# Optimization experiments

Measured on AMD Instinct MI355X. Metric: run time of the kernel, lower is better.

## Reference

```python
import jax, jax.numpy as jnp
import numpy as np
from math import sqrt

D_MODEL, D_COND, N_HEADS = 512, 768, 8
B, H, W, L_COND = 8, 64, 64, 256


def setup_inputs() -> dict:
    key = jax.random.key(0)
    ks = jax.random.split(key, 7)
    return {
        "image": jax.random.normal(ks[0], (B, D_MODEL, H, W), jnp.float32),
        "cond": jax.random.normal(ks[1], (B, L_COND, D_COND), jnp.float32),
        "attention_mask": jnp.zeros((B, H * W, L_COND), jnp.float32),
        "Wq": jax.random.normal(ks[2], (D_MODEL, D_MODEL), jnp.float32) * 0.02,
        "Wk": jax.random.normal(ks[3], (D_MODEL, D_COND), jnp.float32) * 0.02,
        "Wv": jax.random.normal(ks[4], (D_MODEL, D_COND), jnp.float32) * 0.02,
        "Wo": jax.random.normal(ks[5], (D_MODEL, D_MODEL), jnp.float32) * 0.02,
        "bo": jnp.zeros((D_MODEL,), jnp.float32),
    }


def reference(image, cond, attention_mask, Wq, Wk, Wv, Wo, bo):
    b, d, h, w = image.shape
    L = h * w
    n = N_HEADS
    dh = d // n
    scale = sqrt(dh)
    # b d h w -> b l d
    x = image.reshape(b, d, L).transpose(0, 2, 1)
    # projections (torch Linear: y = x @ W.T), split heads: b l (n dh) -> b n l dh
    q = (x @ Wq.T).reshape(b, L, n, dh).transpose(0, 2, 1, 3)
    k = (cond @ Wk.T).reshape(b, -1, n, dh).transpose(0, 2, 1, 3)
    v = (cond @ Wv.T).reshape(b, -1, n, dh).transpose(0, 2, 1, 3)
    attn = jnp.einsum("bnqd,bnkd->bnqk", q, k) / scale
    attn = attn + attention_mask[:, None]  # b 1 L L_cond
    p = jax.nn.softmax(attn, axis=-1)
    o = jnp.einsum("bnqk,bnkd->bnqd", p, v)  # b n L dh
    # b n (h w) dh -> b (n dh) h w
    o = o.transpose(0, 1, 3, 2).reshape(b, d, h, w)
    # 1x1 conv == per-pixel linear over channels
    out = jnp.einsum("oc,bchw->bohw", Wo, o) + bo[None, :, None, None]
    return out
```

## Files before the change

kernel.cpp:

```cpp
#include <hip/hip_runtime.h>

typedef __bf16 bf16x8 __attribute__((ext_vector_type(8)));
typedef float f32x4 __attribute__((ext_vector_type(4)));
typedef short s4 __attribute__((ext_vector_type(4)));
typedef unsigned short ush;

#define DEV __device__ __forceinline__


DEV ush f2bf(float x){
  union { float f; unsigned u; } v; v.f = x;
  unsigned r = v.u + 0x7FFFu + ((v.u >> 16) & 1u);
  return (ush)(r >> 16);
}

DEV short bfcast(float x){
  union { __bf16 h; short s; } cv; cv.h = (__bf16)x; return cv.s;
}

DEV void gload_lds16(const ush* g, ush* l){
  __builtin_amdgcn_global_load_lds(
      (const __attribute__((address_space(1))) unsigned int*)g,
      (__attribute__((address_space(3))) unsigned int*)l, 16, 0, 0);
}

__global__ __launch_bounds__(256) void tc_kernel(const float* __restrict__ img, ush* __restrict__ xT){
  __shared__ float tile[32][33];
  const int b = blockIdx.z;
  const int l0 = blockIdx.x << 5, c0 = blockIdx.y << 5;
  const int tx = threadIdx.x & 31, ty = threadIdx.x >> 5;
  const float* src = img + ((size_t)b*512 + c0)*4096 + l0;
  #pragma unroll
  for (int i = 0; i < 32; i += 8) tile[ty+i][tx] = src[(size_t)(ty+i)*4096 + tx];
  __syncthreads();
  ush* dst = xT + ((size_t)b*4096 + l0)*512 + c0;
  #pragma unroll
  for (int i = 0; i < 32; i += 8) dst[(size_t)(ty+i)*512 + tx] = f2bf(tile[tx][ty+i]);
}

__global__ __launch_bounds__(256) void cvt_kernel(const float* c0,const float* c1,const float* c2,
                                                  const float* c3,const float* c4,
                                                  ush* o0, ush* o1, ush* o2, ush* o3, ush* o4){
  const int N0=1572864, N1=262144, N2=393216, N3=393216, N4=262144;
  const int stride = gridDim.x * blockDim.x;
  for (int i = blockIdx.x*blockDim.x + threadIdx.x; i < N0+N1+N2+N3+N4; i += stride){
    int j = i; const float* s; ush* d;
    if (j < N0){ s=c0; d=o0; }
    else { j-=N0; if (j<N1){s=c1;d=o1;}
      else { j-=N1; if (j<N2){s=c2;d=o2;}
        else { j-=N2; if (j<N3){s=c3;d=o3;} else { j-=N3; s=c4; d=o4; } } } }
    d[j] = f2bf(s[j]);
  }
}

DEV void gemm_core(const ush* __restrict__ Ag, long long a_row0, int lda,
                   const ush* __restrict__ Bg, long long b_row0, int ldb,
                   int K, ush* As, ush* Bs, f32x4 acc[4][4])
{
  const int t = threadIdx.x;
  const int lane = t & 63;
  const int wid = t >> 6, wr = wid >> 1, wc = wid & 1;
  #pragma unroll
  for (int mt=0;mt<4;mt++)
    #pragma unroll
    for (int nt=0;nt<4;nt++) acc[mt][nt] = f32x4{0.f,0.f,0.f,0.f};

  const int nk = K >> 6;
  for (int kt = 0; kt < nk; ++kt){
    const int k0 = kt << 6;
    #pragma unroll
    for (int r = 0; r < 4; ++r){
      int idx = (r<<8) + t;
      int row = idx >> 3, slot = idx & 7;
      gload_lds16(Ag + (a_row0 + row)*(long long)lda + k0 + ((slot ^ (row&7))<<3), As + idx*8);
    }
    #pragma unroll
    for (int r = 0; r < 4; ++r){
      int idx = (r<<8) + t;
      int row = idx >> 3, slot = idx & 7;
      gload_lds16(Bg + (b_row0 + row)*(long long)ldb + k0 + ((slot ^ (row&7))<<3), Bs + idx*8);
    }
    __syncthreads();
    #pragma unroll
    for (int kk = 0; kk < 2; ++kk){
      bf16x8 af[4], bfv[4];
      #pragma unroll
      for (int mt=0;mt<4;mt++){
        int row = (wr<<6) + (mt<<4) + (lane & 15);
        int byte = (row<<7) + (kk<<6) + ((lane>>4)<<4);
        byte ^= (row & 7) << 4;
        af[mt] = *(const bf16x8*)((const char*)As + byte);
      }
      #pragma unroll
      for (int nt=0;nt<4;nt++){
        int row = (wc<<6) + (nt<<4) + (lane & 15);
        int byte = (row<<7) + (kk<<6) + ((lane>>4)<<4);
        byte ^= (row & 7) << 4;
        bfv[nt] = *(const bf16x8*)((const char*)Bs + byte);
      }
      #pragma unroll
      for (int mt=0;mt<4;mt++)
        #pragma unroll
        for (int nt=0;nt<4;nt++)
          acc[mt][nt] = __builtin_amdgcn_mfma_f32_16x16x32_bf16(af[mt], bfv[nt], acc[mt][nt], 0,0,0);
    }
    __syncthreads();
  }
}

__global__ __launch_bounds__(256,2) void qproj_kernel(const ush* __restrict__ xT, const ush* __restrict__ Wqb,
                                                      ush* __restrict__ Qg){
  __shared__ ush As[8192], Bs[8192];
  f32x4 acc[4][4];
  const int nb = blockIdx.x & 3, mb = blockIdx.x >> 2;
  gemm_core(xT, (long long)mb*128, 512, Wqb, (long long)nb*128, 512, 512, As, Bs, acc);
  const int lane = threadIdx.x & 63, wid = threadIdx.x >> 6, wr = wid>>1, wc = wid&1;
  #pragma unroll
  for (int mt=0;mt<4;mt++)
    #pragma unroll
    for (int nt=0;nt<4;nt++)
      #pragma unroll
      for (int r=0;r<4;r++){
        int m = mb*128 + (wr<<6) + (mt<<4) + ((lane>>4)<<2) + r;
        int n = (nb<<7) + (wc<<6) + (nt<<4) + (lane&15);
        int bb = m >> 12, l = m & 4095, hh = n >> 6, dh = n & 63;
        Qg[(((size_t)(bb*8 + hh)*4096 + l)<<6) + dh] = f2bf(acc[mt][nt][r] * 0.125f);
      }
}

__global__ __launch_bounds__(256,2) void kvproj_kernel(const ush* __restrict__ cb, const ush* __restrict__ Wkb,
                                                       const ush* __restrict__ Wvb, ush* __restrict__ Kg,
                                                       ush* __restrict__ Vt){
  __shared__ ush As[8192], Bs[8192];
  f32x4 acc[4][4];
  const int which = blockIdx.z;
  const int nb = blockIdx.x & 3, mb = blockIdx.x >> 2;
  gemm_core(cb, (long long)mb*128, 768, which ? Wvb : Wkb, (long long)nb*128, 768, 768, As, Bs, acc);
  const int lane = threadIdx.x & 63, wid = threadIdx.x >> 6, wr = wid>>1, wc = wid&1;
  #pragma unroll
  for (int mt=0;mt<4;mt++)
    #pragma unroll
    for (int nt=0;nt<4;nt++)
      #pragma unroll
      for (int r=0;r<4;r++){
        int m = mb*128 + (wr<<6) + (mt<<4) + ((lane>>4)<<2) + r;
        int n = (nb<<7) + (wc<<6) + (nt<<4) + (lane&15);
        int bb = m >> 8, j = m & 255;
        ush val = f2bf(acc[mt][nt][r]);
        if (!which) Kg[(((size_t)(bb*256 + j))<<9) + n] = val;
        else { int hh = n>>6, dh = n&63; Vt[(((size_t)((bb*8+hh)*64 + dh))<<8) + j] = val; }
      }
}

__global__ __launch_bounds__(1024,3) void attn_kernel(const ush* __restrict__ Qg, const ush* __restrict__ Kg,
                                                      const ush* __restrict__ Vg, const float* __restrict__ mask,
                                                      ush* __restrict__ Oc){
  extern __shared__ char smem[];
  ush* Ks = (ush*)smem;
  ush* Vs = (ush*)(smem + 32768);
  const int t = threadIdx.x, lane = t & 63, wid = t >> 6;
  const int qb = blockIdx.x, h = blockIdx.y, b = blockIdx.z;

  #pragma unroll
  for (int r = 0; r < 2; ++r){
    int idx = (r<<10) + t;
    int j = idx >> 3, slot = idx & 7;
    gload_lds16(Kg + ((size_t)(b*256 + j))*512 + h*64 + ((slot ^ (j&7))<<3), Ks + idx*8);
  }
  #pragma unroll
  for (int r = 0; r < 2; ++r){
    int idx = (r<<10) + t;
    int dh = idx >> 5, slot = idx & 31;
    gload_lds16(Vg + ((size_t)((b*8 + h)*64 + dh))*256 + ((((slot&7) ^ (dh&7)) | (slot&24))<<3), Vs + idx*8);
  }
  __syncthreads();

  const int l15 = lane & 15, kg = lane >> 4;
  const ush* Qbase = Qg + ((size_t)(b*8 + h)*4096)*64;
  const int q00 = qb*1024 + wid*64;

  #pragma unroll 1
  for (int mp = 0; mp < 2; ++mp){
    const int qA = q00 + mp*32 + l15;
    const int qB = qA + 16;
    bf16x8 qf00 = *(const bf16x8*)(Qbase + (size_t)qA*64 + (kg<<3));
    bf16x8 qf01 = *(const bf16x8*)(Qbase + (size_t)qA*64 + 32 + (kg<<3));
    bf16x8 qf10 = *(const bf16x8*)(Qbase + (size_t)qB*64 + (kg<<3));
    bf16x8 qf11 = *(const bf16x8*)(Qbase + (size_t)qB*64 + 32 + (kg<<3));
    const float* mrowA = mask + ((size_t)b*4096 + qA)*256 + (kg<<2);
    const float* mrowB = mrowA + (16<<8);

    f32x4 oaccA[4], oaccB[4];
    #pragma unroll
    for (int tl=0;tl<4;++tl){ oaccA[tl] = f32x4{0.f,0.f,0.f,0.f}; oaccB[tl] = f32x4{0.f,0.f,0.f,0.f}; }
    float mA = 0.f, mB = 0.f;
    f32x4 svA = f32x4{0.f,0.f,0.f,0.f}, svB = f32x4{0.f,0.f,0.f,0.f};

    #pragma unroll 1
    for (int qt = 0; qt < 4; ++qt){
      f32x4 sA[4], sB[4];
      #pragma unroll
      for (int nt=0;nt<4;++nt){ sA[nt] = f32x4{0.f,0.f,0.f,0.f}; sB[nt] = f32x4{0.f,0.f,0.f,0.f}; }
      #pragma unroll
      for (int nt=0;nt<4;++nt){
        int row = (qt<<6) + (nt<<4) + l15;
        const char* kb = (const char*)Ks + (row<<7);
        int sw = (row&7)<<4;
        bf16x8 kf0 = *(const bf16x8*)(kb + ((kg<<4) ^ sw));
        bf16x8 kf1 = *(const bf16x8*)(kb + (((kg<<4)+64) ^ sw));
        sA[nt] = __builtin_amdgcn_mfma_f32_16x16x32_bf16(kf0, qf00, sA[nt], 0,0,0);
        sA[nt] = __builtin_amdgcn_mfma_f32_16x16x32_bf16(kf1, qf01, sA[nt], 0,0,0);
        sB[nt] = __builtin_amdgcn_mfma_f32_16x16x32_bf16(kf0, qf10, sB[nt], 0,0,0);
        sB[nt] = __builtin_amdgcn_mfma_f32_16x16x32_bf16(kf1, qf11, sB[nt], 0,0,0);
      }

      float mxA = -3.0e38f, mxB = -3.0e38f;
      #pragma unroll
      for (int nt=0;nt<4;++nt){
        float4 va = *(const float4*)(mrowA + (qt<<6) + (nt<<4));
        float4 vb = *(const float4*)(mrowB + (qt<<6) + (nt<<4));
        sA[nt][0]+=va.x; sA[nt][1]+=va.y; sA[nt][2]+=va.z; sA[nt][3]+=va.w;
        sB[nt][0]+=vb.x; sB[nt][1]+=vb.y; sB[nt][2]+=vb.z; sB[nt][3]+=vb.w;
        #pragma unroll
        for (int r=0;r<4;++r){ mxA = fmaxf(mxA, sA[nt][r]); mxB = fmaxf(mxB, sB[nt][r]); }
      }
      mxA = fmaxf(mxA, __shfl_xor(mxA, 16, 64));
      mxA = fmaxf(mxA, __shfl_xor(mxA, 32, 64));
      mxB = fmaxf(mxB, __shfl_xor(mxB, 16, 64));
      mxB = fmaxf(mxB, __shfl_xor(mxB, 32, 64));

      if (qt == 0){
        mA = mxA; mB = mxB;
      } else {
        float mnA = fmaxf(mA, mxA), mnB = fmaxf(mB, mxB);
        float aA = __expf(mA - mnA), aB = __expf(mB - mnB);
        #pragma unroll
        for (int r=0;r<4;++r){ svA[r] *= aA; svB[r] *= aB; }
        #pragma unroll
        for (int tl=0;tl<4;++tl)
          #pragma unroll
          for (int r=0;r<4;++r){ oaccA[tl][r] *= aA; oaccB[tl][r] *= aB; }
        mA = mnA; mB = mnB;
      }

      #pragma unroll
      for (int nt=0;nt<4;++nt){
        s4 pA, pB;
        #pragma unroll
        for (int r=0;r<4;++r){
          float pa = __expf(sA[nt][r] - mA);
          float pb = __expf(sB[nt][r] - mB);
          svA[r] += pa; svB[r] += pb;
          pA[r] = bfcast(pa); pB[r] = bfcast(pb);
        }
        #pragma unroll
        for (int tl=0;tl<4;++tl){
          int dr = (tl<<4) + l15;
          int off = ((qt<<7) + (nt<<5) + (kg<<3)) ^ ((dr&7)<<4);
          s4 vf = *(const s4*)((const char*)Vs + (dr<<9) + off);
          oaccA[tl] = __builtin_amdgcn_mfma_f32_16x16x16bf16_1k(vf, pA, oaccA[tl], 0,0,0);
          oaccB[tl] = __builtin_amdgcn_mfma_f32_16x16x16bf16_1k(vf, pB, oaccB[tl], 0,0,0);
        }
      }
      __builtin_amdgcn_sched_barrier(0);
    }

    float sAt = (svA[0]+svA[1]) + (svA[2]+svA[3]);
    float sBt = (svB[0]+svB[1]) + (svB[2]+svB[3]);
    sAt += __shfl_xor(sAt, 16, 64); sAt += __shfl_xor(sAt, 32, 64);
    sBt += __shfl_xor(sBt, 16, 64); sBt += __shfl_xor(sBt, 32, 64);
    const float rlA = 1.f / sAt, rlB = 1.f / sBt;
    #pragma unroll
    for (int tl=0;tl<4;++tl){
      s4 ovA, ovB;
      #pragma unroll
      for (int r=0;r<4;++r){ ovA[r] = bfcast(oaccA[tl][r] * rlA); ovB[r] = bfcast(oaccB[tl][r] * rlB); }
      *(s4*)(Oc + (((size_t)b*4096 + qA)<<9) + h*64 + (tl<<4) + (kg<<2)) = ovA;
      *(s4*)(Oc + (((size_t)b*4096 + qB)<<9) + h*64 + (tl<<4) + (kg<<2)) = ovB;
    }
  }
}

__global__ __launch_bounds__(256,2) void oproj_kernel(const ush* __restrict__ Wob, const ush* __restrict__ Oc,
                                                      const float* __restrict__ bo, float* __restrict__ out){
  __shared__ ush As[8192], Bs[8192];
  f32x4 acc[4][4];
  const int bz = blockIdx.z;
  const int mb = blockIdx.x >> 5, nb = blockIdx.x & 31;
  gemm_core(Wob, (long long)mb*128, 512, Oc + (size_t)bz*4096*512, (long long)nb*128, 512, 512, As, Bs, acc);
  const int lane = threadIdx.x & 63, wid = threadIdx.x >> 6, wr = wid>>1, wc = wid&1;
  #pragma unroll
  for (int mt=0;mt<4;mt++)
    #pragma unroll
    for (int nt=0;nt<4;nt++){
      #pragma unroll
      for (int r=0;r<4;r++){
        int m = (mb<<7) + (wr<<6) + (mt<<4) + ((lane>>4)<<2) + r;
        int n = (nb<<7) + (wc<<6) + (nt<<4) + (lane&15);
        out[(((size_t)(bz*512 + m))<<12) + n] = acc[mt][nt][r] + bo[m];
      }
    }
}

extern "C" void kernel_launch(void* const* d_in, const int* in_sizes, int n_in,
                              void* d_out, int out_size, void* d_ws, size_t ws_size,
                              hipStream_t stream){
  const float* image = (const float*)d_in[0];
  const float* cond  = (const float*)d_in[1];
  const float* mask  = (const float*)d_in[2];
  const float* Wq    = (const float*)d_in[3];
  const float* Wk    = (const float*)d_in[4];
  const float* Wv    = (const float*)d_in[5];
  const float* Wo    = (const float*)d_in[6];
  const float* bo    = (const float*)d_in[7];
  float* out = (float*)d_out;

  char* ws = (char*)d_ws;
  ush* xT   = (ush*)(ws);
  ush* Oc   = xT;
  ush* Qg   = (ush*)(ws + 33554432);
  ush* cndb = (ush*)(ws + 67108864);
  ush* Kg   = (ush*)(ws + 70254592);
  ush* Vt   = (ush*)(ws + 72351744);
  ush* Wqb  = (ush*)(ws + 74448896);
  ush* Wkb  = (ush*)(ws + 74973184);
  ush* Wvb  = (ush*)(ws + 75759616);
  ush* Wob  = (ush*)(ws + 76546048);

  (void)hipFuncSetAttribute((const void*)attn_kernel,
                            hipFuncAttributeMaxDynamicSharedMemorySize, 65536);

  tc_kernel<<<dim3(128,16,8), 256, 0, stream>>>(image, xT);
  cvt_kernel<<<dim3(1024), 256, 0, stream>>>(cond, Wq, Wk, Wv, Wo, cndb, Wqb, Wkb, Wvb, Wob);
  qproj_kernel<<<dim3(1024), 256, 0, stream>>>(xT, Wqb, Qg);
  kvproj_kernel<<<dim3(64,1,2), 256, 0, stream>>>(cndb, Wkb, Wvb, Kg, Vt);
  attn_kernel<<<dim3(4,8,8), 1024, 65536, stream>>>(Qg, Kg, Vt, mask, Oc);
  oproj_kernel<<<dim3(128,1,8), 256, 0, stream>>>(Wob, Oc, bo, out);
}
```

Before: 159.0 us.

## Use exp2 softmax with lazy rescale, permuted V layout, and rotated key tiles

Folds log2(e) into the Q scale and mask add so the softmax uses exp2f directly. Running-max rescaling is skipped unless a wave's max grows by more than 8. V is stored in a permuted column order so each lane fetches its P·V operand with two 16-byte LDS reads instead of four 8-byte reads. Key-tile order is rotated per wave to spread LDS bank traffic, and s_setprio brackets the MFMA sections. The lazy rescale lets unnormalised exponentials grow up to 2^8 before correction, which bf16 P and fp32 accumulators must absorb.

Result: no change. 161.4 us (+1.5%).

```diff
diff --git a/kernel.cpp b/kernel.cpp
--- a/kernel.cpp
+++ b/kernel.cpp
@@ -3,6 +3,7 @@
 typedef __bf16 bf16x8 __attribute__((ext_vector_type(8)));
 typedef float f32x4 __attribute__((ext_vector_type(4)));
 typedef short s4 __attribute__((ext_vector_type(4)));
+typedef short s8 __attribute__((ext_vector_type(8)));
 typedef unsigned short ush;
 
 #define DEV __device__ __forceinline__
@@ -124,7 +125,7 @@
         int m = mb*128 + (wr<<6) + (mt<<4) + ((lane>>4)<<2) + r;
         int n = (nb<<7) + (wc<<6) + (nt<<4) + (lane&15);
         int bb = m >> 12, l = m & 4095, hh = n >> 6, dh = n & 63;
-        Qg[(((size_t)(bb*8 + hh)*4096 + l)<<6) + dh] = f2bf(acc[mt][nt][r] * 0.125f);
+        Qg[(((size_t)(bb*8 + hh)*4096 + l)<<6) + dh] = f2bf(acc[mt][nt][r] * 0.180336880f);
       }
 }
 
@@ -148,7 +149,11 @@
         int bb = m >> 8, j = m & 255;
         ush val = f2bf(acc[mt][nt][r]);
         if (!which) Kg[(((size_t)(bb*256 + j))<<9) + n] = val;
-        else { int hh = n>>6, dh = n&63; Vt[(((size_t)((bb*8+hh)*64 + dh))<<8) + j] = val; }
+        else {
+          int hh = n>>6, dh = n&63;
+          int jp = (j & 0xC3) | (((j>>4)&3)<<2) | (((j>>2)&3)<<4);
+          Vt[(((size_t)((bb*8+hh)*64 + dh))<<8) + jp] = val;
+        }
       }
 }
 
@@ -160,6 +165,7 @@
   ush* Vs = (ush*)(smem + 32768);
   const int t = threadIdx.x, lane = t & 63, wid = t >> 6;
   const int qb = blockIdx.x, h = blockIdx.y, b = blockIdx.z;
+  const float L2E = 1.44269504f;
 
   #pragma unroll
   for (int r = 0; r < 2; ++r){
@@ -178,6 +184,7 @@
   const int l15 = lane & 15, kg = lane >> 4;
   const ush* Qbase = Qg + ((size_t)(b*8 + h)*4096)*64;
   const int q00 = qb*1024 + wid*64;
+  const int rot = wid & 3;
 
   #pragma unroll 1
   for (int mp = 0; mp < 2; ++mp){
@@ -197,10 +204,12 @@
     f32x4 svA = f32x4{0.f,0.f,0.f,0.f}, svB = f32x4{0.f,0.f,0.f,0.f};
 
     #pragma unroll 1
-    for (int qt = 0; qt < 4; ++qt){
+    for (int qq = 0; qq < 4; ++qq){
+      const int qt = (qq + rot) & 3;
       f32x4 sA[4], sB[4];
       #pragma unroll
       for (int nt=0;nt<4;++nt){ sA[nt] = f32x4{0.f,0.f,0.f,0.f}; sB[nt] = f32x4{0.f,0.f,0.f,0.f}; }
+      __builtin_amdgcn_s_setprio(1);
       #pragma unroll
       for (int nt=0;nt<4;++nt){
         int row = (qt<<6) + (nt<<4) + l15;
@@ -213,14 +222,17 @@
         sB[nt] = __builtin_amdgcn_mfma_f32_16x16x32_bf16(kf0, qf10, sB[nt], 0,0,0);
         sB[nt] = __builtin_amdgcn_mfma_f32_16x16x32_bf16(kf1, qf11, sB[nt], 0,0,0);
       }
+      __builtin_amdgcn_s_setprio(0);
 
       float mxA = -3.0e38f, mxB = -3.0e38f;
       #pragma unroll
       for (int nt=0;nt<4;++nt){
         float4 va = *(const float4*)(mrowA + (qt<<6) + (nt<<4));
         float4 vb = *(const float4*)(mrowB + (qt<<6) + (nt<<4));
-        sA[nt][0]+=va.x; sA[nt][1]+=va.y; sA[nt][2]+=va.z; sA[nt][3]+=va.w;
-        sB[nt][0]+=vb.x; sB[nt][1]+=vb.y; sB[nt][2]+=vb.z; sB[nt][3]+=vb.w;
+        sA[nt][0] = fmaf(va.x, L2E, sA[nt][0]); sA[nt][1] = fmaf(va.y, L2E, sA[nt][1]);
+        sA[nt][2] = fmaf(va.z, L2E, sA[nt][2]); sA[nt][3] = fmaf(va.w, L2E, sA[nt][3]);
+        sB[nt][0] = fmaf(vb.x, L2E, sB[nt][0]); sB[nt][1] = fmaf(vb.y, L2E, sB[nt][1]);
+        sB[nt][2] = fmaf(vb.z, L2E, sB[nt][2]); sB[nt][3] = fmaf(vb.w, L2E, sB[nt][3]);
         #pragma unroll
         for (int r=0;r<4;++r){ mxA = fmaxf(mxA, sA[nt][r]); mxB = fmaxf(mxB, sB[nt][r]); }
       }
@@ -229,11 +241,11 @@
       mxB = fmaxf(mxB, __shfl_xor(mxB, 16, 64));
       mxB = fmaxf(mxB, __shfl_xor(mxB, 32, 64));
 
-      if (qt == 0){
+      if (qq == 0){
         mA = mxA; mB = mxB;
-      } else {
+      } else if (!__all(fmaxf(mxA - mA, mxB - mB) <= 8.f)){
         float mnA = fmaxf(mA, mxA), mnB = fmaxf(mB, mxB);
-        float aA = __expf(mA - mnA), aB = __expf(mB - mnB);
+        float aA = exp2f(mA - mnA), aB = exp2f(mB - mnB);
         #pragma unroll
         for (int r=0;r<4;++r){ svA[r] *= aA; svB[r] *= aB; }
         #pragma unroll
@@ -243,25 +255,39 @@
         mA = mnA; mB = mnB;
       }
 
-      #pragma unroll
-      for (int nt=0;nt<4;++nt){
-        s4 pA, pB;
+      s4 pA[4], pB[4];
+      #pragma unroll
+      for (int nt=0;nt<4;++nt)
         #pragma unroll
         for (int r=0;r<4;++r){
-          float pa = __expf(sA[nt][r] - mA);
-          float pb = __expf(sB[nt][r] - mB);
+          float pa = exp2f(sA[nt][r] - mA);
+          float pb = exp2f(sB[nt][r] - mB);
           svA[r] += pa; svB[r] += pb;
-          pA[r] = bfcast(pa); pB[r] = bfcast(pb);
+          pA[nt][r] = bfcast(pa); pB[nt][r] = bfcast(pb);
         }
-        #pragma unroll
-        for (int tl=0;tl<4;++tl){
-          int dr = (tl<<4) + l15;
-          int off = ((qt<<7) + (nt<<5) + (kg<<3)) ^ ((dr&7)<<4);
-          s4 vf = *(const s4*)((const char*)Vs + (dr<<9) + off);
-          oaccA[tl] = __builtin_amdgcn_mfma_f32_16x16x16bf16_1k(vf, pA, oaccA[tl], 0,0,0);
-          oaccB[tl] = __builtin_amdgcn_mfma_f32_16x16x16bf16_1k(vf, pB, oaccB[tl], 0,0,0);
-        }
-      }
+
+      __builtin_amdgcn_s_setprio(1);
+      #pragma unroll
+      for (int tl=0;tl<4;++tl){
+        int dr = (tl<<4) + l15;
+        const char* vb = (const char*)Vs + (dr<<9);
+        int sw = (dr&7)<<4;
+        s8 v01 = *(const s8*)(vb + (((qt<<7)+(kg<<5)) ^ sw));
+        s8 v23 = *(const s8*)(vb + (((qt<<7)+(kg<<5)+16) ^ sw));
+        s4 f0 = __builtin_shufflevector(v01, v01, 0,1,2,3);
+        s4 f1 = __builtin_shufflevector(v01, v01, 4,5,6,7);
+        s4 f2 = __builtin_shufflevector(v23, v23, 0,1,2,3);
+        s4 f3 = __builtin_shufflevector(v23, v23, 4,5,6,7);
+        oaccA[tl] = __builtin_amdgcn_mfma_f32_16x16x16bf16_1k(f0, pA[0], oaccA[tl], 0,0,0);
+        oaccA[tl] = __builtin_amdgcn_mfma_f32_16x16x16bf16_1k(f1, pA[1], oaccA[tl], 0,0,0);
+        oaccA[tl] = __builtin_amdgcn_mfma_f32_16x16x16bf16_1k(f2, pA[2], oaccA[tl], 0,0,0);
+        oaccA[tl] = __builtin_amdgcn_mfma_f32_16x16x16bf16_1k(f3, pA[3], oaccA[tl], 0,0,0);
+        oaccB[tl] = __builtin_amdgcn_mfma_f32_16x16x16bf16_1k(f0, pB[0], oaccB[tl], 0,0,0);
+        oaccB[tl] = __builtin_amdgcn_mfma_f32_16x16x16bf16_1k(f1, pB[1], oaccB[tl], 0,0,0);
+        oaccB[tl] = __builtin_amdgcn_mfma_f32_16x16x16bf16_1k(f2, pB[2], oaccB[tl], 0,0,0);
+        oaccB[tl] = __builtin_amdgcn_mfma_f32_16x16x16bf16_1k(f3, pB[3], oaccB[tl], 0,0,0);
+      }
+      __builtin_amdgcn_s_setprio(0);
       __builtin_amdgcn_sched_barrier(0);
     }
 
```
